# Kernel tuning notes

Hardware: AMD Instinct MI355X
Metric: run time of the kernel (lower is better)

## Reference

```python
import jax, jax.numpy as jnp
import numpy as np

LN_EPS = 1e-5

def _layernorm(x, g, b):
    mu = jnp.mean(x, axis=-1, keepdims=True)
    var = jnp.mean(jnp.square(x - mu), axis=-1, keepdims=True)
    return (x - mu) * jax.lax.rsqrt(var + LN_EPS) * g + b

def setup_inputs() -> dict:
    key = jax.random.key(0)
    ks = jax.random.split(key, 12)
    N0, N1, D0, D1, DO, E = 50000, 50000, 256, 512, 256, 1600000
    return {
        "x0": jax.random.normal(ks[0], (N0, D0), jnp.float32),
        "x1": jax.random.normal(ks[1], (N1, D1), jnp.float32),
        "W0": jax.random.normal(ks[2], (D0, DO), jnp.float32) * 0.05,
        "W1": jax.random.normal(ks[3], (D1, DO), jnp.float32) * 0.05,
        "Wres1": jax.random.normal(ks[4], (D1, DO), jnp.float32) * 0.05,
        "g0": jnp.ones((DO,), jnp.float32),
        "b0": jnp.zeros((DO,), jnp.float32),
        "g1": jnp.ones((DO,), jnp.float32),
        "b1": jnp.zeros((DO,), jnp.float32),
        "ew0": jax.random.uniform(ks[5], (E,), jnp.float32),
        "ew1": jax.random.uniform(ks[6], (E,), jnp.float32),
        "row0": jax.random.randint(ks[7], (E,), 0, N0, jnp.int32),
        "col0": jax.random.randint(ks[8], (E,), 0, N0, jnp.int32),
        "row1": jax.random.randint(ks[9], (E,), 0, N1, jnp.int32),
        "col1": jax.random.randint(ks[10], (E,), 0, N1, jnp.int32),
    }

def _gcn_type(x, W, ew, row, col, g, b, res):
    # h_proj = x @ W ; h_agg[i] = sum_{e: row_e=i} ew_e * h_proj[col_e]  (== spmm(adj, h_proj))
    h_proj = x @ W
    msgs = ew[:, None] * h_proj[col]                      # [E, DO] gather + scale
    h_agg = jax.ops.segment_sum(msgs, row, num_segments=x.shape[0])
    return _layernorm(h_agg + res, g, b)

def reference(x0, x1, W0, W1, Wres1, g0, b0, g1, b1, ew0, ew1, row0, col0, row1, col1):
    out0 = _gcn_type(x0, W0, ew0, row0, col0, g0, b0, x0)          # identity residual
    out1 = _gcn_type(x1, W1, ew1, row1, col1, g1, b1, x1 @ Wres1)  # projected residual
    return jnp.concatenate([out0, out1], axis=0)
```

## Files before the change

### kernel.cpp

```cpp
#include <hip/hip_runtime.h>
#include <hip/hip_bf16.h>
#include <cstddef>

typedef unsigned short u16;
typedef u16 u16x8 __attribute__((ext_vector_type(8)));
typedef __bf16 bf16x8 __attribute__((ext_vector_type(8)));
typedef float f32x4 __attribute__((ext_vector_type(4)));

__device__ __forceinline__ u16 f2b(float f) {
  unsigned int u = __float_as_uint(f);
  unsigned int r = 0x7FFFu + ((u >> 16) & 1u);
  return (u16)((u + r) >> 16);
}
__device__ __forceinline__ float b2f(u16 u) {
  return __uint_as_float(((unsigned int)u) << 16);
}

template <bool OUT_BF16>
__global__ __launch_bounds__(256) void gemm_bf16(
    const float* __restrict__ A, const u16* __restrict__ Bt, void* __restrict__ Cv,
    int M, int K) {
  __shared__ u16 As[64 * 64];
  __shared__ u16 Bs[256 * 64];
  const int tid = threadIdx.x;
  const int wid = tid >> 6;
  const int lane = tid & 63;
  const int brow = blockIdx.x * 64;
  const int waveN = wid * 64;
  const int q = lane >> 4;
  const int rl = lane & 15;

  f32x4 acc[4][4] = {};

  const int arow = tid >> 2;
  const int kq = (tid & 3) * 16;
  const int garow = brow + arow;
  const bool aok = garow < M;
  const int aswz = arow & 7;
  const int brb = tid;
  const int bswz = brb & 7;

  for (int k0 = 0; k0 < K; k0 += 64) {
    {
      const float* src = A + (size_t)garow * K + k0 + kq;
      u16* dstrow = As + arow * 64;
#pragma unroll
      for (int j = 0; j < 2; ++j) {
        float4 v0 = make_float4(0.f, 0.f, 0.f, 0.f), v1 = v0;
        if (aok) {
          v0 = *(const float4*)(src + j * 8);
          v1 = *(const float4*)(src + j * 8 + 4);
        }
        u16x8 v = {f2b(v0.x), f2b(v0.y), f2b(v0.z), f2b(v0.w),
                   f2b(v1.x), f2b(v1.y), f2b(v1.z), f2b(v1.w)};
        const int c = (kq >> 3) + j;
        *(u16x8*)(dstrow + 8 * (c ^ aswz)) = v;
      }
    }
    {
      const u16* src = Bt + (size_t)brb * K + k0;
      u16* dstrow = Bs + brb * 64;
#pragma unroll
      for (int j = 0; j < 8; ++j) {
        u16x8 v = *(const u16x8*)(src + j * 8);
        *(u16x8*)(dstrow + 8 * (j ^ bswz)) = v;
      }
    }
    __syncthreads();
#pragma unroll
    for (int ks = 0; ks < 2; ++ks) {
      bf16x8 af[4], bfr[4];
      const int cbase = ks * 4 + q;
#pragma unroll
      for (int i = 0; i < 4; ++i) {
        const int r = 16 * i + rl;
        af[i] = __builtin_bit_cast(bf16x8,
                 *(const u16x8*)(As + r * 64 + 8 * (cbase ^ (rl & 7))));
      }
#pragma unroll
      for (int j = 0; j < 4; ++j) {
        const int r = waveN + 16 * j + rl;
        bfr[j] = __builtin_bit_cast(bf16x8,
                  *(const u16x8*)(Bs + r * 64 + 8 * (cbase ^ (rl & 7))));
      }
#pragma unroll
      for (int i = 0; i < 4; ++i)
#pragma unroll
        for (int j = 0; j < 4; ++j)
          acc[i][j] = __builtin_amdgcn_mfma_f32_16x16x32_bf16(af[i], bfr[j], acc[i][j], 0, 0, 0);
    }
    __syncthreads();
  }

#pragma unroll
  for (int i = 0; i < 4; ++i) {
#pragma unroll
    for (int reg = 0; reg < 4; ++reg) {
      const int gr = brow + 16 * i + q * 4 + reg;
      if (gr >= M) continue;
#pragma unroll
      for (int j = 0; j < 4; ++j) {
        const int col = waveN + 16 * j + rl;
        const float v = acc[i][j][reg];
        if (OUT_BF16) ((u16*)Cv)[(size_t)gr * 256 + col] = f2b(v);
        else          ((float*)Cv)[(size_t)gr * 256 + col] = v;
      }
    }
  }
}

__global__ __launch_bounds__(256) void conv_wt(const float* __restrict__ W,
                                               u16* __restrict__ Wt, int K) {
  const int idx = blockIdx.x * 256 + threadIdx.x;
  const int k = idx >> 8;
  const int n = idx & 255;
  if (k < K) Wt[(size_t)n * K + k] = f2b(W[idx]);
}

#define EB   256
#define RPB  128
#define NBUK 391

__global__ __launch_bounds__(256) void pa_hist(const int* __restrict__ row,
                                               int* __restrict__ ghist, int E) {
  __shared__ int h[NBUK];
  for (int i = threadIdx.x; i < NBUK; i += 256) h[i] = 0;
  __syncthreads();
  const int per = (E + EB - 1) / EB;
  const int s = blockIdx.x * per;
  const int e = min(E, s + per);
  for (int i = s + threadIdx.x; i < e; i += 256) atomicAdd(&h[row[i] >> 7], 1);
  __syncthreads();
  for (int i = threadIdx.x; i < NBUK; i += 256) ghist[i * EB + blockIdx.x] = h[i];
}

__global__ __launch_bounds__(256) void pa_scatter(
    const int* __restrict__ row, const int* __restrict__ col, const float* __restrict__ ew,
    const int* __restrict__ gscan, int2* __restrict__ tmp, int E) {
  __shared__ int cur[NBUK];
  for (int i = threadIdx.x; i < NBUK; i += 256) cur[i] = gscan[i * EB + blockIdx.x];
  __syncthreads();
  const int per = (E + EB - 1) / EB;
  const int s = blockIdx.x * per;
  const int e = min(E, s + per);
  for (int i0 = s + threadIdx.x; i0 < e; i0 += 1024) {
    int r[4], c[4], wv[4];
    bool ok[4];
#pragma unroll
    for (int j = 0; j < 4; ++j) {
      const int i = i0 + j * 256;
      ok[j] = i < e;
      if (ok[j]) { r[j] = row[i]; c[j] = col[i]; wv[j] = __float_as_int(ew[i]); }
    }
#pragma unroll
    for (int j = 0; j < 4; ++j)
      if (ok[j]) {
        const int pos = atomicAdd(&cur[r[j] >> 7], 1);
        tmp[pos] = make_int2(((r[j] & 127) << 16) | c[j], wv[j]);
      }
  }
}

__global__ __launch_bounds__(256) void pb_sort(
    const int2* __restrict__ tmp, const int* __restrict__ gscan,
    int2* __restrict__ sedge, int* __restrict__ offs, int E, int N) {
  __shared__ int h[RPB];
  __shared__ int ex[RPB];
  __shared__ int cur[RPB];
  const int b = blockIdx.x;
  const int t = threadIdx.x;
  const int base = gscan[b * EB];
  const int end = (b == NBUK - 1) ? E : gscan[(b + 1) * EB];
  if (t < RPB) h[t] = 0;
  __syncthreads();
  for (int i = base + t; i < end; i += 256) atomicAdd(&h[(tmp[i].x >> 16) & 127], 1);
  __syncthreads();
  if (t == 0) {
    int run = base;
    for (int r = 0; r < RPB; ++r) { const int cc = h[r]; ex[r] = run; cur[r] = run; run += cc; }
  }
  __syncthreads();
  if (t < RPB) {
    const int rg = b * RPB + t;
    if (rg <= N) offs[rg] = ex[t];
  }
  for (int i = base + t; i < end; i += 256) {
    const int2 v = tmp[i];
    const int pos = atomicAdd(&cur[(v.x >> 16) & 127], 1);
    sedge[pos] = make_int2(v.x & 0xFFFF, v.y);
  }
}

__global__ __launch_bounds__(256) void scan1(const int* __restrict__ deg,
                                             int* __restrict__ offs,
                                             int* __restrict__ partials, int n) {
  __shared__ int sh[256];
  const int t = threadIdx.x;
  const int base = blockIdx.x * 1024 + t * 4;
  int v[4];
#pragma unroll
  for (int j = 0; j < 4; j++) v[j] = (base + j < n) ? deg[base + j] : 0;
  const int tsum = v[0] + v[1] + v[2] + v[3];
  sh[t] = tsum;
  __syncthreads();
  for (int off = 1; off < 256; off <<= 1) {
    int x = (t >= off) ? sh[t - off] : 0;
    __syncthreads();
    sh[t] += x;
    __syncthreads();
  }
  if (t == 255) partials[blockIdx.x] = sh[255];
  int run = sh[t] - tsum;
#pragma unroll
  for (int j = 0; j < 4; j++) {
    if (base + j < n) offs[base + j] = run;
    run += v[j];
  }
}

__global__ void scan2(int* __restrict__ partials, int nb) {
  if (threadIdx.x == 0 && blockIdx.x == 0) {
    int run = 0;
    for (int i = 0; i < nb; i++) {
      int t = partials[i];
      partials[i] = run;
      run += t;
    }
  }
}

__global__ __launch_bounds__(256) void scan_add(int* __restrict__ a,
                                                const int* __restrict__ partials, int n) {
  const int t = threadIdx.x;
  const int base = blockIdx.x * 1024 + t * 4;
  const int add = partials[blockIdx.x];
#pragma unroll
  for (int j = 0; j < 4; j++)
    if (base + j < n) a[base + j] += add;
}

__global__ __launch_bounds__(256) void agg_ln(
    const u16* __restrict__ hpb, const int* __restrict__ offs,
    const int2* __restrict__ sedge,
    const float* __restrict__ res, const float* __restrict__ g, const float* __restrict__ b,
    float* __restrict__ out, int nrows) {
  const int wave = threadIdx.x >> 6;
  const int lane = threadIdx.x & 63;
  const int r = blockIdx.x * 4 + wave;
  if (r >= nrows) return;
  const int half = lane >> 5;
  const int f8 = (lane & 31) * 8;

  float acc8[8] = {0.f, 0.f, 0.f, 0.f, 0.f, 0.f, 0.f, 0.f};
  int k = offs[r];
  const int kend = offs[r + 1];
  for (; k + 7 < kend; k += 8) {
    int2 e[4];
#pragma unroll
    for (int j = 0; j < 4; ++j) e[j] = sedge[k + half + 2 * j];
    u16x8 h[4];
#pragma unroll
    for (int j = 0; j < 4; ++j)
      h[j] = *(const u16x8*)(hpb + (size_t)e[j].x * 256 + f8);
#pragma unroll
    for (int j = 0; j < 4; ++j) {
      const float w = __int_as_float(e[j].y);
#pragma unroll
      for (int d = 0; d < 8; ++d) acc8[d] += w * b2f(h[j][d]);
    }
  }
  for (int kc = k + half; kc < kend; kc += 2) {
    const int2 e = sedge[kc];
    const float w = __int_as_float(e.y);
    const u16x8 h = *(const u16x8*)(hpb + (size_t)e.x * 256 + f8);
#pragma unroll
    for (int d = 0; d < 8; ++d) acc8[d] += w * b2f(h[d]);
  }

#pragma unroll
  for (int d = 0; d < 8; ++d) acc8[d] += __shfl_xor(acc8[d], 32);

  {
    const float4 r0 = *(const float4*)(res + (size_t)r * 256 + f8);
    const float4 r1 = *(const float4*)(res + (size_t)r * 256 + f8 + 4);
    acc8[0] += r0.x; acc8[1] += r0.y; acc8[2] += r0.z; acc8[3] += r0.w;
    acc8[4] += r1.x; acc8[5] += r1.y; acc8[6] += r1.z; acc8[7] += r1.w;
  }

  float s = 0.f;
#pragma unroll
  for (int d = 0; d < 8; ++d) s += acc8[d];
#pragma unroll
  for (int m = 32; m >= 1; m >>= 1) s += __shfl_xor(s, m);
  const float mu = s * (1.f / 512.f);
#pragma unroll
  for (int d = 0; d < 8; ++d) acc8[d] -= mu;
  float ss = 0.f;
#pragma unroll
  for (int d = 0; d < 8; ++d) ss += acc8[d] * acc8[d];
#pragma unroll
  for (int m = 32; m >= 1; m >>= 1) ss += __shfl_xor(ss, m);
  const float rs = rsqrtf(ss * (1.f / 512.f) + 1e-5f);

  if (half == 0) {
    const float4 g0v = *(const float4*)(g + f8);
    const float4 g1v = *(const float4*)(g + f8 + 4);
    const float4 b0v = *(const float4*)(b + f8);
    const float4 b1v = *(const float4*)(b + f8 + 4);
    float4 o0, o1;
    o0.x = acc8[0] * rs * g0v.x + b0v.x;
    o0.y = acc8[1] * rs * g0v.y + b0v.y;
    o0.z = acc8[2] * rs * g0v.z + b0v.z;
    o0.w = acc8[3] * rs * g0v.w + b0v.w;
    o1.x = acc8[4] * rs * g1v.x + b1v.x;
    o1.y = acc8[5] * rs * g1v.y + b1v.y;
    o1.z = acc8[6] * rs * g1v.z + b1v.z;
    o1.w = acc8[7] * rs * g1v.w + b1v.w;
    *(float4*)(out + (size_t)r * 256 + f8) = o0;
    *(float4*)(out + (size_t)r * 256 + f8 + 4) = o1;
  }
}

extern "C" void kernel_launch(void* const* d_in, const int* in_sizes, int n_in,
                              void* d_out, int out_size, void* d_ws, size_t ws_size,
                              hipStream_t stream) {
  const float* x0    = (const float*)d_in[0];
  const float* x1    = (const float*)d_in[1];
  const float* W0    = (const float*)d_in[2];
  const float* W1    = (const float*)d_in[3];
  const float* Wres1 = (const float*)d_in[4];
  const float* g0    = (const float*)d_in[5];
  const float* b0    = (const float*)d_in[6];
  const float* g1    = (const float*)d_in[7];
  const float* b1    = (const float*)d_in[8];
  const float* ew0   = (const float*)d_in[9];
  const float* ew1   = (const float*)d_in[10];
  const int*   row0  = (const int*)d_in[11];
  const int*   col0  = (const int*)d_in[12];
  const int*   row1  = (const int*)d_in[13];
  const int*   col1  = (const int*)d_in[14];
  float* out = (float*)d_out;

  const int N = 50000, D0 = 256, D1 = 512, DO = 256, E = 1600000;

  char* w = (char*)d_ws;
  u16*   hpb   = (u16*)  (w);
  u16*   wtb   = (u16*)  (w + 25600000);
  int2*  sedge = (int2*) (w + 25862144);
  int*   offs  = (int*)  (w + 38662144);
  int*   ghist = (int*)  (w + 38862160);
  int*   parts = (int*)  (w + 39262560);
  int2*  tmp   = (int2*) (w);

  float* out0 = out;
  float* out1 = out + (size_t)N * DO;

  const dim3 blk(256);
  const dim3 gemm_grid((N + 63) / 64);
  const dim3 agg_grid((N + 3) / 4);
  const int NGH = NBUK * EB;
  const int NBS = (NGH + 1023) / 1024;

  auto build_csr = [&](const int* row, const int* col, const float* ew) {
    pa_hist<<<dim3(EB), blk, 0, stream>>>(row, ghist, E);
    scan1<<<dim3(NBS), blk, 0, stream>>>(ghist, ghist, parts, NGH);
    scan2<<<dim3(1), dim3(64), 0, stream>>>(parts, NBS);
    scan_add<<<dim3(NBS), blk, 0, stream>>>(ghist, parts, NGH);
    pa_scatter<<<dim3(EB), blk, 0, stream>>>(row, col, ew, ghist, tmp, E);
    pb_sort<<<dim3(NBUK), blk, 0, stream>>>(tmp, ghist, sedge, offs, E, N);
  };

  build_csr(row0, col0, ew0);
  conv_wt<<<dim3(D0), blk, 0, stream>>>(W0, wtb, D0);
  gemm_bf16<true><<<gemm_grid, blk, 0, stream>>>(x0, wtb, hpb, N, D0);
  agg_ln<<<agg_grid, blk, 0, stream>>>(hpb, offs, sedge, x0, g0, b0, out0, N);

  conv_wt<<<dim3(D1), blk, 0, stream>>>(Wres1, wtb, D1);
  gemm_bf16<false><<<gemm_grid, blk, 0, stream>>>(x1, wtb, out1, N, D1);
  build_csr(row1, col1, ew1);
  conv_wt<<<dim3(D1), blk, 0, stream>>>(W1, wtb, D1);
  gemm_bf16<true><<<gemm_grid, blk, 0, stream>>>(x1, wtb, hpb, N, D1);
  agg_ln<<<agg_grid, blk, 0, stream>>>(hpb, offs, sedge, out1, g1, b1, out1, N);
}
```

Baseline: 707.4 us.

## Vectorize edge-partition loads, parallelize bucket scan, deepen aggregation unroll, add nontemporal hints

The histogram and scatter kernels now read row/col/ew four at a time as nontemporal vector loads, and block edge ranges are padded to multiples of four so the loads stay aligned. The serial single-thread exclusive scan in the per-bucket sort is replaced by a parallel Hillis-Steele scan in shared memory. The aggregation kernel adds a 16-edge unrolled loop so more gathers are in flight, and uses nontemporal loads for edges and residuals and nontemporal stores for the output. These changes target memory latency and cache pollution in a bandwidth-bound pipeline, at the cost of more registers per thread in the aggregation kernel.

```diff
diff --git a/kernel.cpp b/kernel.cpp
--- a/kernel.cpp
+++ b/kernel.cpp
@@ -6,6 +6,8 @@
 typedef u16 u16x8 __attribute__((ext_vector_type(8)));
 typedef __bf16 bf16x8 __attribute__((ext_vector_type(8)));
 typedef float f32x4 __attribute__((ext_vector_type(4)));
+typedef int i32x4 __attribute__((ext_vector_type(4)));
+typedef float f32x4v __attribute__((ext_vector_type(4)));
 
 __device__ __forceinline__ u16 f2b(float f) {
   unsigned int u = __float_as_uint(f);
@@ -121,15 +123,28 @@
 #define RPB  128
 #define NBUK 391
 
+__device__ __forceinline__ void edge_range(int E, int blk, int& s, int& e) {
+  const int per = (((E + EB - 1) / EB) + 3) & ~3;
+  s = blk * per;
+  e = min(E, s + per);
+}
+
 __global__ __launch_bounds__(256) void pa_hist(const int* __restrict__ row,
                                                int* __restrict__ ghist, int E) {
   __shared__ int h[NBUK];
   for (int i = threadIdx.x; i < NBUK; i += 256) h[i] = 0;
   __syncthreads();
-  const int per = (E + EB - 1) / EB;
-  const int s = blockIdx.x * per;
-  const int e = min(E, s + per);
-  for (int i = s + threadIdx.x; i < e; i += 256) atomicAdd(&h[row[i] >> 7], 1);
+  int s, e;
+  edge_range(E, blockIdx.x, s, e);
+  for (int i = s + threadIdx.x * 4; i < e; i += 1024) {
+    if (i + 3 < e) {
+      const i32x4 rr = __builtin_nontemporal_load((const i32x4*)(row + i));
+#pragma unroll
+      for (int j = 0; j < 4; ++j) atomicAdd(&h[rr[j] >> 7], 1);
+    } else {
+      for (int i2 = i; i2 < e; ++i2) atomicAdd(&h[row[i2] >> 7], 1);
+    }
+  }
   __syncthreads();
   for (int i = threadIdx.x; i < NBUK; i += 256) ghist[i * EB + blockIdx.x] = h[i];
 }
@@ -140,24 +155,25 @@
   __shared__ int cur[NBUK];
   for (int i = threadIdx.x; i < NBUK; i += 256) cur[i] = gscan[i * EB + blockIdx.x];
   __syncthreads();
-  const int per = (E + EB - 1) / EB;
-  const int s = blockIdx.x * per;
-  const int e = min(E, s + per);
-  for (int i0 = s + threadIdx.x; i0 < e; i0 += 1024) {
-    int r[4], c[4], wv[4];
-    bool ok[4];
-#pragma unroll
-    for (int j = 0; j < 4; ++j) {
-      const int i = i0 + j * 256;
-      ok[j] = i < e;
-      if (ok[j]) { r[j] = row[i]; c[j] = col[i]; wv[j] = __float_as_int(ew[i]); }
-    }
-#pragma unroll
-    for (int j = 0; j < 4; ++j)
-      if (ok[j]) {
-        const int pos = atomicAdd(&cur[r[j] >> 7], 1);
-        tmp[pos] = make_int2(((r[j] & 127) << 16) | c[j], wv[j]);
-      }
+  int s, e;
+  edge_range(E, blockIdx.x, s, e);
+  for (int i0 = s + threadIdx.x * 4; i0 < e; i0 += 1024) {
+    if (i0 + 3 < e) {
+      const i32x4 r4 = __builtin_nontemporal_load((const i32x4*)(row + i0));
+      const i32x4 c4 = __builtin_nontemporal_load((const i32x4*)(col + i0));
+      const f32x4 w4 = __builtin_nontemporal_load((const f32x4*)(ew + i0));
+#pragma unroll
+      for (int j = 0; j < 4; ++j) {
+        const int pos = atomicAdd(&cur[r4[j] >> 7], 1);
+        tmp[pos] = make_int2(((r4[j] & 127) << 16) | c4[j], __float_as_int(w4[j]));
+      }
+    } else {
+      for (int i2 = i0; i2 < e; ++i2) {
+        const int r = row[i2];
+        const int pos = atomicAdd(&cur[r >> 7], 1);
+        tmp[pos] = make_int2(((r & 127) << 16) | col[i2], __float_as_int(ew[i2]));
+      }
+    }
   }
 }
 
@@ -165,7 +181,7 @@
     const int2* __restrict__ tmp, const int* __restrict__ gscan,
     int2* __restrict__ sedge, int* __restrict__ offs, int E, int N) {
   __shared__ int h[RPB];
-  __shared__ int ex[RPB];
+  __shared__ int sc[RPB];
   __shared__ int cur[RPB];
   const int b = blockIdx.x;
   const int t = threadIdx.x;
@@ -175,15 +191,21 @@
   __syncthreads();
   for (int i = base + t; i < end; i += 256) atomicAdd(&h[(tmp[i].x >> 16) & 127], 1);
   __syncthreads();
-  if (t == 0) {
-    int run = base;
-    for (int r = 0; r < RPB; ++r) { const int cc = h[r]; ex[r] = run; cur[r] = run; run += cc; }
-  }
-  __syncthreads();
+  if (t < RPB) sc[t] = h[t];
+  __syncthreads();
+  for (int off = 1; off < RPB; off <<= 1) {
+    int x = (t >= off && t < RPB) ? sc[t - off] : 0;
+    __syncthreads();
+    if (t < RPB) sc[t] += x;
+    __syncthreads();
+  }
   if (t < RPB) {
+    const int ex = base + sc[t] - h[t];
+    cur[t] = ex;
     const int rg = b * RPB + t;
-    if (rg <= N) offs[rg] = ex[t];
-  }
+    if (rg <= N) offs[rg] = ex;
+  }
+  __syncthreads();
   for (int i = base + t; i < end; i += 256) {
     const int2 v = tmp[i];
     const int pos = atomicAdd(&cur[(v.x >> 16) & 127], 1);
@@ -250,29 +272,48 @@
   if (r >= nrows) return;
   const int half = lane >> 5;
   const int f8 = (lane & 31) * 8;
+  const long long* sedge8 = (const long long*)sedge;
 
   float acc8[8] = {0.f, 0.f, 0.f, 0.f, 0.f, 0.f, 0.f, 0.f};
   int k = offs[r];
   const int kend = offs[r + 1];
+
+  for (; k + 15 < kend; k += 16) {
+    long long e[8];
+#pragma unroll
+    for (int j = 0; j < 8; ++j)
+      e[j] = __builtin_nontemporal_load(sedge8 + k + half + 2 * j);
+    u16x8 h[8];
+#pragma unroll
+    for (int j = 0; j < 8; ++j)
+      h[j] = *(const u16x8*)(hpb + (size_t)(int)(e[j] & 0xFFFFFFFFll) * 256 + f8);
+#pragma unroll
+    for (int j = 0; j < 8; ++j) {
+      const float w = __int_as_float((int)(e[j] >> 32));
+#pragma unroll
+      for (int d = 0; d < 8; ++d) acc8[d] += w * b2f(h[j][d]);
+    }
+  }
   for (; k + 7 < kend; k += 8) {
-    int2 e[4];
-#pragma unroll
-    for (int j = 0; j < 4; ++j) e[j] = sedge[k + half + 2 * j];
+    long long e[4];
+#pragma unroll
+    for (int j = 0; j < 4; ++j)
+      e[j] = __builtin_nontemporal_load(sedge8 + k + half + 2 * j);
     u16x8 h[4];
 #pragma unroll
     for (int j = 0; j < 4; ++j)
-      h[j] = *(const u16x8*)(hpb + (size_t)e[j].x * 256 + f8);
+      h[j] = *(const u16x8*)(hpb + (size_t)(int)(e[j] & 0xFFFFFFFFll) * 256 + f8);
 #pragma unroll
     for (int j = 0; j < 4; ++j) {
-      const float w = __int_as_float(e[j].y);
+      const float w = __int_as_float((int)(e[j] >> 32));
 #pragma unroll
       for (int d = 0; d < 8; ++d) acc8[d] += w * b2f(h[j][d]);
     }
   }
   for (int kc = k + half; kc < kend; kc += 2) {
-    const int2 e = sedge[kc];
-    const float w = __int_as_float(e.y);
-    const u16x8 h = *(const u16x8*)(hpb + (size_t)e.x * 256 + f8);
+    const long long e = sedge8[kc];
+    const float w = __int_as_float((int)(e >> 32));
+    const u16x8 h = *(const u16x8*)(hpb + (size_t)(int)(e & 0xFFFFFFFFll) * 256 + f8);
 #pragma unroll
     for (int d = 0; d < 8; ++d) acc8[d] += w * b2f(h[d]);
   }
@@ -281,10 +322,10 @@
   for (int d = 0; d < 8; ++d) acc8[d] += __shfl_xor(acc8[d], 32);
 
   {
-    const float4 r0 = *(const float4*)(res + (size_t)r * 256 + f8);
-    const float4 r1 = *(const float4*)(res + (size_t)r * 256 + f8 + 4);
-    acc8[0] += r0.x; acc8[1] += r0.y; acc8[2] += r0.z; acc8[3] += r0.w;
-    acc8[4] += r1.x; acc8[5] += r1.y; acc8[6] += r1.z; acc8[7] += r1.w;
+    const f32x4 r0 = __builtin_nontemporal_load((const f32x4*)(res + (size_t)r * 256 + f8));
+    const f32x4 r1 = __builtin_nontemporal_load((const f32x4*)(res + (size_t)r * 256 + f8 + 4));
+#pragma unroll
+    for (int d = 0; d < 4; ++d) { acc8[d] += r0[d]; acc8[4 + d] += r1[d]; }
   }
 
   float s = 0.f;
@@ -307,17 +348,17 @@
     const float4 g1v = *(const float4*)(g + f8 + 4);
     const float4 b0v = *(const float4*)(b + f8);
     const float4 b1v = *(const float4*)(b + f8 + 4);
-    float4 o0, o1;
-    o0.x = acc8[0] * rs * g0v.x + b0v.x;
-    o0.y = acc8[1] * rs * g0v.y + b0v.y;
-    o0.z = acc8[2] * rs * g0v.z + b0v.z;
-    o0.w = acc8[3] * rs * g0v.w + b0v.w;
-    o1.x = acc8[4] * rs * g1v.x + b1v.x;
-    o1.y = acc8[5] * rs * g1v.y + b1v.y;
-    o1.z = acc8[6] * rs * g1v.z + b1v.z;
-    o1.w = acc8[7] * rs * g1v.w + b1v.w;
-    *(float4*)(out + (size_t)r * 256 + f8) = o0;
-    *(float4*)(out + (size_t)r * 256 + f8 + 4) = o1;
+    f32x4 o0, o1;
+    o0[0] = acc8[0] * rs * g0v.x + b0v.x;
+    o0[1] = acc8[1] * rs * g0v.y + b0v.y;
+    o0[2] = acc8[2] * rs * g0v.z + b0v.z;
+    o0[3] = acc8[3] * rs * g0v.w + b0v.w;
+    o1[0] = acc8[4] * rs * g1v.x + b1v.x;
+    o1[1] = acc8[5] * rs * g1v.y + b1v.y;
+    o1[2] = acc8[6] * rs * g1v.z + b1v.z;
+    o1[3] = acc8[7] * rs * g1v.w + b1v.w;
+    __builtin_nontemporal_store(o0, (f32x4*)(out + (size_t)r * 256 + f8));
+    __builtin_nontemporal_store(o1, (f32x4*)(out + (size_t)r * 256 + f8 + 4));
   }
 }
 
```

Measured after the change: 694.5 us. Within noise of the previous version (-1.8%).
